# Performance work log

Measured on AMD Instinct MI355X. Metric: run time of the kernel, lower is better.

## Reference

```python
import jax, jax.numpy as jnp
import numpy as np


def setup_inputs() -> dict:
    key = jax.random.key(0)
    k1, k2, k3 = jax.random.split(key, 3)
    B, S, D_IN, D_OUT = 4, 2048, 4096, 4096
    x = jax.random.normal(k1, (B, S, D_IN), dtype=jnp.float32)
    # int8 quantized weight, stored as int8 (values in [-127, 127])
    weight = jax.random.randint(k2, (D_OUT, D_IN), -127, 128, dtype=jnp.int8)
    weight_scaler = jax.random.uniform(k3, (D_OUT,), dtype=jnp.float32) * 0.02
    return {"x": x, "weight": weight, "weight_scaler": weight_scaler}


def reference(x, weight, weight_scaler):
    # quant path: dequantize weight with per-output-channel scale, then F.linear
    w = weight.astype(jnp.float32) * weight_scaler[:, None]  # [D_OUT, D_IN]
    # F.linear(x, w) == x @ w.T
    return jnp.einsum('bsd,od->bso', x, w)
```

## Files before the change

### kernel.cpp

```cpp
#include <hip/hip_runtime.h>
#include <cstdint>
#include <cstddef>

typedef int i32x4 __attribute__((ext_vector_type(4)));

static __device__ __forceinline__ int pack4(float4 v, float inv) {
  int a = __float2int_rn(v.x * inv) & 0xFF;
  int b = __float2int_rn(v.y * inv) & 0xFF;
  int c = __float2int_rn(v.z * inv) & 0xFF;
  int d = __float2int_rn(v.w * inv) & 0xFF;
  return a | (b << 8) | (c << 16) | (d << 24);
}

__global__ __launch_bounds__(256) void prep_fast(
    const float* __restrict__ x, signed char* __restrict__ xq, float* __restrict__ xs,
    const int* __restrict__ w, signed char* __restrict__ wq,
    int xblocks) {
  const int t = threadIdx.x;
  if ((int)blockIdx.x < xblocks) {
    const int lane = t & 63;
    const int row  = ((int)blockIdx.x << 2) + (t >> 6);
    const float4* xr = (const float4*)(x + ((size_t)row << 12));
    float4 v[16];
#pragma unroll
    for (int i = 0; i < 16; ++i) v[i] = xr[(i << 6) + lane];
    float amax = 0.f;
#pragma unroll
    for (int i = 0; i < 16; ++i)
      amax = fmaxf(amax, fmaxf(fmaxf(fabsf(v[i].x), fabsf(v[i].y)),
                               fmaxf(fabsf(v[i].z), fabsf(v[i].w))));
#pragma unroll
    for (int off = 32; off > 0; off >>= 1)
      amax = fmaxf(amax, __shfl_xor(amax, off, 64));
    const float inv = (amax > 0.f) ? 127.f / amax : 0.f;
    if (lane == 0) xs[row] = amax / 127.f;
    int* o = (int*)(xq + ((size_t)row << 12));
#pragma unroll
    for (int i = 0; i < 16; ++i) o[(i << 6) + lane] = pack4(v[i], inv);
  } else {
    const size_t base = (((size_t)blockIdx.x - xblocks) << 10) + t;
    const int4* wp = (const int4*)w;
    int* op = (int*)wq;
#pragma unroll
    for (int i = 0; i < 4; ++i) {
      int4 vv = wp[base + (i << 8)];
      op[base + (i << 8)] = (vv.x & 0xFF) | ((vv.y & 0xFF) << 8) |
                            ((vv.z & 0xFF) << 16) | ((vv.w & 0xFF) << 24);
    }
  }
}

__global__ __launch_bounds__(256) void prep_kernel(
    const float* __restrict__ x, signed char* __restrict__ xq, float* __restrict__ xs,
    const int* __restrict__ w, signed char* __restrict__ wq,
    int K, int xrows) {
  const int t = threadIdx.x;
  if ((int)blockIdx.x < xrows) {
    const int row = blockIdx.x;
    const float4* xr = (const float4*)(x + (size_t)row * K);
    const int n4 = K >> 2;
    __shared__ float wmax[4];
    float amax = 0.f;
    for (int i = t; i < n4; i += 256) {
      float4 v = xr[i];
      amax = fmaxf(amax, fmaxf(fmaxf(fabsf(v.x), fabsf(v.y)),
                               fmaxf(fabsf(v.z), fabsf(v.w))));
    }
#pragma unroll
    for (int off = 32; off > 0; off >>= 1)
      amax = fmaxf(amax, __shfl_xor(amax, off, 64));
    if ((t & 63) == 0) wmax[t >> 6] = amax;
    __syncthreads();
    amax = fmaxf(fmaxf(wmax[0], wmax[1]), fmaxf(wmax[2], wmax[3]));
    const float inv = (amax > 0.f) ? 127.f / amax : 0.f;
    if (t == 0) xs[row] = amax / 127.f;
    int* o = (int*)(xq + (size_t)row * K);
    for (int i = t; i < n4; i += 256) {
      float4 v = xr[i];
      o[i] = pack4(v, inv);
    }
  } else {
    const size_t g = (size_t)(blockIdx.x - xrows) * 256 + t;
    int4 v = ((const int4*)w)[g];
    ((int*)wq)[g] = (v.x & 0xFF) | ((v.y & 0xFF) << 8) |
                    ((v.z & 0xFF) << 16) | ((v.w & 0xFF) << 24);
  }
}

static __device__ __forceinline__ void gld_lds16(const void* g, void* l) {
  __builtin_amdgcn_global_load_lds(
      (const __attribute__((address_space(1))) unsigned int*)g,
      (__attribute__((address_space(3))) unsigned int*)l,
      16, 0, 0);
}

__global__ __launch_bounds__(512, 2) void gemm_i8_ds(
    const signed char* __restrict__ A,
    const signed char* __restrict__ B,
    const float* __restrict__ xs,
    const float* __restrict__ ws,
    float* __restrict__ C,
    int M, int N, int K) {
  __shared__ __align__(16) signed char lds[131072];

  const int tid  = threadIdx.x;
  const int lane = tid & 63;
  const int wave = tid >> 6;
  const int wm   = wave >> 2;
  const int wn   = wave & 3;
  const int q    = lane >> 4;
  const int r16  = lane & 15;
  const int e    = lane & 7;

  const unsigned nwg = gridDim.x * gridDim.y;
  unsigned id = blockIdx.y * gridDim.x + blockIdx.x;
  if ((nwg & 7u) == 0u) id = (id & 7u) * (nwg >> 3) + (id >> 3);
  const int m0 = (int)(id / gridDim.x) << 8;
  const int n0 = (int)(id % gridDim.x) << 8;

  const int NT = K >> 7;

  const int srow   = tid >> 3;
  const int schunk = ((tid & 7) ^ (srow & 7)) << 4;
  const signed char* sA = A + (size_t)(m0 + srow) * K + schunk;
  const signed char* sB = B + (size_t)(n0 + srow) * K + schunk;
  signed char* lW = lds + wave * 1024;

  const int aro = ((wm << 4) + r16) << 7;
  const int bro = r16 << 7;
  const int cs  = (q ^ e) << 4;

  i32x4 acc[8][4];
#pragma unroll
  for (int i = 0; i < 8; ++i)
#pragma unroll
    for (int j = 0; j < 4; ++j) acc[i][j] = (i32x4){0, 0, 0, 0};
  i32x4 af[4][2], bf[2][2][2];

#define STAGE(Tv, Gv)                                                        \
  do {                                                                       \
    const int t_ = (Tv);                                                     \
    if (t_ < NT) {                                                           \
      const int mat_ = (Gv) & 1, half_ = (Gv) >> 1;                          \
      signed char* l_ = lW + ((t_ & 1) << 15) + (mat_ << 16) + (half_ << 14);\
      const signed char* g_ = (mat_ ? sB : sA) +                             \
                              (size_t)(half_ << 7) * K + ((size_t)t_ << 7);  \
      gld_lds16(g_, l_);                                                     \
      gld_lds16(g_ + (size_t)64 * K, l_ + 8192);                             \
    }                                                                        \
  } while (0)

#define READ_A(MH)                                                           \
  _Pragma("unroll") for (int i_ = 0; i_ < 4; ++i_)                           \
    _Pragma("unroll") for (int kh_ = 0; kh_ < 2; ++kh_)                      \
      af[i_][kh_] = *(const i32x4*)(pA + ((((MH) << 2) + i_) << 12) + aro +  \
                                    (cs ^ (kh_ << 6)));

#define READ_B                                                               \
  _Pragma("unroll") for (int nh_ = 0; nh_ < 2; ++nh_)                        \
    _Pragma("unroll") for (int j_ = 0; j_ < 2; ++j_)                         \
      _Pragma("unroll") for (int kh_ = 0; kh_ < 2; ++kh_)                    \
        bf[nh_][j_][kh_] = *(const i32x4*)(pB + (nh_ << 14) + (wn << 12) +   \
                                           (j_ << 11) + bro + (cs ^ (kh_ << 6)));

#define MFMA_HALF(MH)                                                        \
  __builtin_amdgcn_s_setprio(1);                                             \
  _Pragma("unroll") for (int kh_ = 0; kh_ < 2; ++kh_)                        \
    _Pragma("unroll") for (int i_ = 0; i_ < 4; ++i_)                         \
      _Pragma("unroll") for (int nh_ = 0; nh_ < 2; ++nh_)                    \
        _Pragma("unroll") for (int j_ = 0; j_ < 2; ++j_)                     \
          acc[((MH) << 2) + i_][(nh_ << 1) + j_] =                           \
              __builtin_amdgcn_mfma_i32_16x16x64_i8(                         \
                  af[i_][kh_], bf[(nh_)][j_][kh_],                           \
                  acc[((MH) << 2) + i_][(nh_ << 1) + j_], 0, 0, 0);          \
  __builtin_amdgcn_s_setprio(0);

  STAGE(0, 0); STAGE(0, 1); STAGE(0, 2); STAGE(0, 3);
  STAGE(1, 0); STAGE(1, 1);
  asm volatile("s_waitcnt vmcnt(4)" ::: "memory");
  __builtin_amdgcn_s_barrier();

  for (int t = 0; t < NT; ++t) {
    const signed char* pA = lds + ((t & 1) << 15);
    const signed char* pB = lds + 65536 + ((t & 1) << 15);
    READ_A(0);
    READ_B;
    STAGE(t + 1, 2); STAGE(t + 1, 3);
    MFMA_HALF(0);
    __builtin_amdgcn_s_barrier();
    READ_A(1);
    STAGE(t + 2, 0); STAGE(t + 2, 1);
    MFMA_HALF(1);
    if (t < NT - 2) asm volatile("s_waitcnt vmcnt(4)" ::: "memory");
    else            asm volatile("s_waitcnt vmcnt(0)" ::: "memory");
    __builtin_amdgcn_s_barrier();
  }
#undef MFMA_HALF
#undef READ_B
#undef READ_A
#undef STAGE

#pragma unroll
  for (int mt = 0; mt < 8; ++mt) {
    const int row0 = m0 + (mt << 5) + (wm << 4) + (q << 2);
    float xv[4];
#pragma unroll
    for (int r = 0; r < 4; ++r) xv[r] = xs[row0 + r];
#pragma unroll
    for (int nt = 0; nt < 4; ++nt) {
      const int col = n0 + ((nt >> 1) << 7) + (wn << 5) + ((nt & 1) << 4) + r16;
      const float s = ws[col];
      float* Cp = C + (size_t)row0 * N + col;
#pragma unroll
      for (int r = 0; r < 4; ++r)
        Cp[(size_t)r * N] = (float)acc[mt][nt][r] * xv[r] * s;
    }
  }
}

__global__ void naive_kernel(const float* __restrict__ x, const int* __restrict__ w,
                             const float* __restrict__ sc, float* __restrict__ out,
                             int M, int N, int K) {
  int idx = blockIdx.x * 256 + threadIdx.x;
  if (idx >= M * N) return;
  int m = idx / N, n = idx % N;
  const float* xr = x + (size_t)m * K;
  const int*   wr = w + (size_t)n * K;
  float acc = 0.f;
  for (int k = 0; k < K; ++k) acc += xr[k] * (float)wr[k];
  out[idx] = acc * sc[n];
}

extern "C" void kernel_launch(void* const* d_in, const int* in_sizes, int n_in,
                              void* d_out, int out_size, void* d_ws, size_t ws_size,
                              hipStream_t stream) {
  const float* x  = (const float*)d_in[0];
  const int*   w  = (const int*)d_in[1];
  const float* sc = (const float*)d_in[2];
  float* out = (float*)d_out;

  const int N = in_sizes[2];
  const int K = in_sizes[1] / N;
  const int M = in_sizes[0] / K;

  const size_t need = (size_t)M * K + (size_t)N * K + (size_t)M * 4 + 16;
  if (ws_size < need || (M & 255) || (N & 255) || (K & 127) || K < 256 ||
      (((size_t)N * K) % 1024)) {
    int total = M * N;
    naive_kernel<<<(total + 255) / 256, 256, 0, stream>>>(x, w, sc, out, M, N, K);
    return;
  }

  signed char* xq = (signed char*)d_ws;
  signed char* wq = xq + (size_t)M * K;
  float*       xsc = (float*)(wq + (size_t)N * K);

  if (K == 4096 && (M & 3) == 0 && (((size_t)N * K) % 4096) == 0) {
    const int xblocks = M >> 2;
    const int wblocks = (int)(((size_t)N * K) >> 12);
    prep_fast<<<xblocks + wblocks, 256, 0, stream>>>(x, xq, xsc, w, wq, xblocks);
  } else {
    const int wblocks = (int)(((size_t)N * K) / 1024);
    prep_kernel<<<M + wblocks, 256, 0, stream>>>(x, xq, xsc, w, wq, K, M);
  }

  dim3 grid(N >> 8, M >> 8);
  gemm_i8_ds<<<grid, 512, 0, stream>>>(xq, wq, xsc, sc, out, M, N, K);
}
```

Before: 382.9 us.

## Restructure int8 GEMM main loop to one barrier per K-tile with interleaved LDS reads

The main loop now issues all four global-to-LDS stages for the next tile at the start of each iteration and keeps a single barrier, preceded by a full vmcnt(0) wait, per iteration. Previously the loop used two barriers per iteration with half-tile staging interleaved two tiles ahead. The second half's A-fragment LDS reads are interleaved between the first half's per-row MFMA groups, with setprio covering the whole MFMA sequence. This removes a barrier and lets LDS reads overlap MFMAs. In exchange, global loads get only one iteration of compute to hide their latency, and the full drain at each iteration end may expose memory stalls.

```diff
diff --git a/kernel.cpp b/kernel.cpp
--- a/kernel.cpp
+++ b/kernel.cpp
@@ -94,7 +94,7 @@
       16, 0, 0);
 }
 
-__global__ __launch_bounds__(512, 2) void gemm_i8_ds(
+__global__ __launch_bounds__(512, 2) void gemm_i8_1b(
     const signed char* __restrict__ A,
     const signed char* __restrict__ B,
     const float* __restrict__ xs,
@@ -156,6 +156,11 @@
       af[i_][kh_] = *(const i32x4*)(pA + ((((MH) << 2) + i_) << 12) + aro +  \
                                     (cs ^ (kh_ << 6)));
 
+#define RDA1(IV)                                                             \
+  _Pragma("unroll") for (int kh_ = 0; kh_ < 2; ++kh_)                        \
+    af[IV][kh_] = *(const i32x4*)(pA + ((4 + (IV)) << 12) + aro +            \
+                                  (cs ^ (kh_ << 6)));
+
 #define READ_B                                                               \
   _Pragma("unroll") for (int nh_ = 0; nh_ < 2; ++nh_)                        \
     _Pragma("unroll") for (int j_ = 0; j_ < 2; ++j_)                         \
@@ -163,40 +168,41 @@
         bf[nh_][j_][kh_] = *(const i32x4*)(pB + (nh_ << 14) + (wn << 12) +   \
                                            (j_ << 11) + bro + (cs ^ (kh_ << 6)));
 
-#define MFMA_HALF(MH)                                                        \
-  __builtin_amdgcn_s_setprio(1);                                             \
+#define MFMA_I(MH, IV)                                                       \
   _Pragma("unroll") for (int kh_ = 0; kh_ < 2; ++kh_)                        \
-    _Pragma("unroll") for (int i_ = 0; i_ < 4; ++i_)                         \
-      _Pragma("unroll") for (int nh_ = 0; nh_ < 2; ++nh_)                    \
-        _Pragma("unroll") for (int j_ = 0; j_ < 2; ++j_)                     \
-          acc[((MH) << 2) + i_][(nh_ << 1) + j_] =                           \
-              __builtin_amdgcn_mfma_i32_16x16x64_i8(                         \
-                  af[i_][kh_], bf[(nh_)][j_][kh_],                           \
-                  acc[((MH) << 2) + i_][(nh_ << 1) + j_], 0, 0, 0);          \
-  __builtin_amdgcn_s_setprio(0);
+    _Pragma("unroll") for (int nh_ = 0; nh_ < 2; ++nh_)                      \
+      _Pragma("unroll") for (int j_ = 0; j_ < 2; ++j_)                       \
+        acc[((MH) << 2) + (IV)][(nh_ << 1) + j_] =                           \
+            __builtin_amdgcn_mfma_i32_16x16x64_i8(                           \
+                af[IV][kh_], bf[nh_][j_][kh_],                               \
+                acc[((MH) << 2) + (IV)][(nh_ << 1) + j_], 0, 0, 0);
 
   STAGE(0, 0); STAGE(0, 1); STAGE(0, 2); STAGE(0, 3);
-  STAGE(1, 0); STAGE(1, 1);
-  asm volatile("s_waitcnt vmcnt(4)" ::: "memory");
+  asm volatile("s_waitcnt vmcnt(0)" ::: "memory");
   __builtin_amdgcn_s_barrier();
 
   for (int t = 0; t < NT; ++t) {
     const signed char* pA = lds + ((t & 1) << 15);
     const signed char* pB = lds + 65536 + ((t & 1) << 15);
+    STAGE(t + 1, 0); STAGE(t + 1, 1); STAGE(t + 1, 2); STAGE(t + 1, 3);
     READ_A(0);
     READ_B;
-    STAGE(t + 1, 2); STAGE(t + 1, 3);
-    MFMA_HALF(0);
+    __builtin_amdgcn_s_setprio(1);
+    MFMA_I(0, 0); RDA1(0);
+    MFMA_I(0, 1); RDA1(1);
+    MFMA_I(0, 2); RDA1(2);
+    MFMA_I(0, 3); RDA1(3);
+    MFMA_I(1, 0);
+    MFMA_I(1, 1);
+    MFMA_I(1, 2);
+    MFMA_I(1, 3);
+    __builtin_amdgcn_s_setprio(0);
+    asm volatile("s_waitcnt vmcnt(0)" ::: "memory");
     __builtin_amdgcn_s_barrier();
-    READ_A(1);
-    STAGE(t + 2, 0); STAGE(t + 2, 1);
-    MFMA_HALF(1);
-    if (t < NT - 2) asm volatile("s_waitcnt vmcnt(4)" ::: "memory");
-    else            asm volatile("s_waitcnt vmcnt(0)" ::: "memory");
-    __builtin_amdgcn_s_barrier();
-  }
-#undef MFMA_HALF
+  }
+#undef MFMA_I
 #undef READ_B
+#undef RDA1
 #undef READ_A
 #undef STAGE
 
@@ -265,5 +271,5 @@
   }
 
   dim3 grid(N >> 8, M >> 8);
-  gemm_i8_ds<<<grid, 512, 0, stream>>>(xq, wq, xsc, sc, out, M, N, K);
-}
+  gemm_i8_1b<<<grid, 512, 0, stream>>>(xq, wq, xsc, sc, out, M, N, K);
+}
```

New measurement: 384.6 us. Within noise of the previous version (+0.5%).
